# Kernel optimization log

Measured on AMD Instinct MI355X. Metric: run time of the kernel, lower is better.

## Reference

```python
import jax, jax.numpy as jnp
import numpy as np

B, T, C, H = 2, 2048, 2048, 16
DH = C // H  # 128
INNER = 4 * C  # 8192
EPS = 1e-5


def _ln(x, w, b):
    mu = jnp.mean(x, axis=-1, keepdims=True)
    var = jnp.mean((x - mu) ** 2, axis=-1, keepdims=True)
    return (x - mu) * jax.lax.rsqrt(var + EPS) * w + b


def _apply_rotary(x, cos, sin):
    # x: [B,H,T,DH]; cos/sin: [T,DH//2] broadcast over B,H
    x1 = x[..., ::2]
    x2 = x[..., 1::2]
    r = jnp.stack([x1 * cos - x2 * sin, x1 * sin + x2 * cos], axis=-1)
    return r.reshape(r.shape[:-2] + (-1,))


def setup_inputs() -> dict:
    key = jax.random.key(0)
    ks = jax.random.split(key, 8)
    std = 0.02
    x = jax.random.normal(ks[0], (B, T, C), dtype=jnp.float32)
    # RoPE tables
    inv_freq = 1.0 / (10000.0 ** (np.arange(0, DH, 2, dtype=np.float32) / DH))
    ang = np.arange(T, dtype=np.float32)[:, None] * inv_freq[None, :]  # [T, DH//2]
    cos = jnp.asarray(np.cos(ang))
    sin = jnp.asarray(np.sin(ang))
    return {
        "x": x,
        "cos": cos,
        "sin": sin,
        "ln1_w": jnp.ones((C,), jnp.float32),
        "ln1_b": jnp.zeros((C,), jnp.float32),
        "ln2_w": jnp.ones((C,), jnp.float32),
        "ln2_b": jnp.zeros((C,), jnp.float32),
        "W_qkv": jax.random.normal(ks[1], (C, 3 * C), jnp.float32) * std,
        "W_o": jax.random.normal(ks[2], (C, C), jnp.float32) * std,
        "W1": jax.random.normal(ks[3], (C, INNER), jnp.float32) * std,
        "W2": jax.random.normal(ks[4], (C, INNER), jnp.float32) * std,
        "W3": jax.random.normal(ks[5], (INNER, C), jnp.float32) * std,
    }


def reference(x, cos, sin, ln1_w, ln1_b, ln2_w, ln2_b, W_qkv, W_o, W1, W2, W3):
    # --- attention sub-block (pre-LN) ---
    a = _ln(x, ln1_w, ln1_b)
    qkv = a @ W_qkv  # [B,T,3C]
    q, k, v = jnp.split(qkv, 3, axis=-1)
    q = q.reshape(B, T, H, DH).transpose(0, 2, 1, 3)  # [B,H,T,DH]
    k = k.reshape(B, T, H, DH).transpose(0, 2, 1, 3)
    v = v.reshape(B, T, H, DH).transpose(0, 2, 1, 3)
    q = _apply_rotary(q, cos, sin)
    k = _apply_rotary(k, cos, sin)
    scores = jnp.einsum("bhtd,bhsd->bhts", q, k) / jnp.sqrt(jnp.float32(DH))
    mask = jnp.triu(jnp.full((T, T), -jnp.inf, dtype=scores.dtype), k=1)
    scores = scores + mask
    attn = jax.nn.softmax(scores, axis=-1)
    y = jnp.einsum("bhts,bhsd->bhtd", attn, v)
    y = y.transpose(0, 2, 1, 3).reshape(B, T, C) @ W_o
    x = x + y
    # --- SwiGLU MLP sub-block (pre-LN) ---
    h = _ln(x, ln2_w, ln2_b)
    m = (jax.nn.silu(h @ W1) * (h @ W2)) @ W3
    return x + m
```

## Files before the change

### kernel.cpp

```cpp
#include <hip/hip_runtime.h>
#include <hip/hip_bf16.h>
#include <cstdint>

#define DEVINL __device__ __forceinline__

using f32x4  = __attribute__((ext_vector_type(4))) float;
using short8 = __attribute__((ext_vector_type(8))) short;
using short4v = __attribute__((ext_vector_type(4))) short;

DEVINL float bf2f(__hip_bfloat16 h){ return __bfloat162float(h); }
DEVINL __hip_bfloat16 f2bf(float f){ return __float2bfloat16(f); }
DEVINL short bfbits(float f){ __hip_bfloat16 h = __float2bfloat16(f); short s; __builtin_memcpy(&s, &h, 2); return s; }
DEVINL float sb2f(short s){ uint32_t u = ((uint32_t)(uint16_t)s) << 16; float f; __builtin_memcpy(&f, &u, 4); return f; }

DEVINL void gl_lds16(const void* g, void* l){
  __builtin_amdgcn_global_load_lds((const __attribute__((address_space(1))) void*)g,
                                   (__attribute__((address_space(3))) void*)l, 16, 0, 0);
}

__global__ __launch_bounds__(256) void wtrans(const float* __restrict__ src,
                                              __hip_bfloat16* __restrict__ dst,
                                              int R, int C){
  __shared__ float tile[32][33];
  const int tr0 = blockIdx.y*32, tc0 = blockIdx.x*32;
  const int t = threadIdx.x;
  const int lr = t >> 3, lc = (t & 7) * 4;
  float4 v = *(const float4*)(src + (size_t)(tr0+lr)*C + tc0 + lc);
  tile[lr][lc] = v.x; tile[lr][lc+1] = v.y; tile[lr][lc+2] = v.z; tile[lr][lc+3] = v.w;
  __syncthreads();
  short4v o;
  o[0] = bfbits(tile[lc+0][lr]);
  o[1] = bfbits(tile[lc+1][lr]);
  o[2] = bfbits(tile[lc+2][lr]);
  o[3] = bfbits(tile[lc+3][lr]);
  *(short4v*)(dst + (size_t)(tc0+lr)*R + tr0 + lc) = o;
}

__global__ __launch_bounds__(256) void ln_k(const float* __restrict__ x,
                                            const float* __restrict__ w,
                                            const float* __restrict__ bia,
                                            __hip_bfloat16* __restrict__ out){
  const int row = blockIdx.x, t = threadIdx.x;
  const float* xr = x + (size_t)row*2048;
  float4 v0 = *(const float4*)(xr + t*4);
  float4 v1 = *(const float4*)(xr + 1024 + t*4);
  float s  = v0.x+v0.y+v0.z+v0.w + v1.x+v1.y+v1.z+v1.w;
  float ss = v0.x*v0.x+v0.y*v0.y+v0.z*v0.z+v0.w*v0.w
           + v1.x*v1.x+v1.y*v1.y+v1.z*v1.z+v1.w*v1.w;
  #pragma unroll
  for (int o=1;o<64;o<<=1){ s += __shfl_xor(s,o); ss += __shfl_xor(ss,o); }
  __shared__ float red[8];
  const int wv = t>>6, ln = t&63;
  if (ln==0){ red[wv]=s; red[4+wv]=ss; }
  __syncthreads();
  s = red[0]+red[1]+red[2]+red[3]; ss = red[4]+red[5]+red[6]+red[7];
  const float mu = s*(1.f/2048.f);
  const float inv = rsqrtf(ss*(1.f/2048.f) - mu*mu + 1e-5f);
  {
    float4 wv4 = *(const float4*)(w + t*4);
    float4 bv4 = *(const float4*)(bia + t*4);
    short4v o;
    o[0]=bfbits((v0.x-mu)*inv*wv4.x + bv4.x);
    o[1]=bfbits((v0.y-mu)*inv*wv4.y + bv4.y);
    o[2]=bfbits((v0.z-mu)*inv*wv4.z + bv4.z);
    o[3]=bfbits((v0.w-mu)*inv*wv4.w + bv4.w);
    *(short4v*)(out + (size_t)row*2048 + t*4) = o;
  }
  {
    float4 wv4 = *(const float4*)(w + 1024 + t*4);
    float4 bv4 = *(const float4*)(bia + 1024 + t*4);
    short4v o;
    o[0]=bfbits((v1.x-mu)*inv*wv4.x + bv4.x);
    o[1]=bfbits((v1.y-mu)*inv*wv4.y + bv4.y);
    o[2]=bfbits((v1.z-mu)*inv*wv4.z + bv4.z);
    o[3]=bfbits((v1.w-mu)*inv*wv4.w + bv4.w);
    *(short4v*)(out + (size_t)row*2048 + 1024 + t*4) = o;
  }
}

template<int EPI, int BM>
__global__ __launch_bounds__(512, 2) void gemmp(
    const __hip_bfloat16* __restrict__ A,
    const __hip_bfloat16* __restrict__ Bt,
    __hip_bfloat16* __restrict__ Cb,
    float* __restrict__ Cf,
    const float* __restrict__ resid,
    const __hip_bfloat16* __restrict__ emul,
    int M, int N, int K, int NTN)
{
  constexpr int MF    = BM/32;
  constexpr int LA    = BM/128;
  constexpr int ABY   = BM*64;
  constexpr int TILEB = ABY + 16384;
  extern __shared__ char smem[];
  const int tid = threadIdx.x, lane = tid & 63, wave = tid >> 6;
  const int l15 = lane & 15, l4 = lane >> 4;
  const int wm = wave >> 2, wn = wave & 3;

  const int nwg = gridDim.x;
  const int id  = blockIdx.x;
  const int swz = (id & 7) * (nwg >> 3) + (id >> 3);
  const int by = swz / NTN, bx = swz % NTN;
  const int row0 = by * BM, col0 = bx * 256;

  const __hip_bfloat16* srcA[LA]; int dstA[LA];
  #pragma unroll
  for (int g = 0; g < LA; ++g){
    const int c = g*512 + tid, r = c >> 2, s = c & 3;
    const int kbyte = (s*16) ^ (((r >> 1) & 3) << 4);
    srcA[g] = A + (size_t)(row0 + r)*K + (kbyte >> 1);
    dstA[g] = c*16;
  }
  const __hip_bfloat16* srcB[2]; int dstB[2];
  #pragma unroll
  for (int g = 0; g < 2; ++g){
    const int c = g*512 + tid, r = c >> 2, s = c & 3;
    const int kbyte = (s*16) ^ (((r >> 1) & 3) << 4);
    srcB[g] = Bt + (size_t)(col0 + r)*K + (kbyte >> 1);
    dstB[g] = c*16;
  }
  auto STAGE = [&](int bi, int kt){
    char* base = smem + bi*TILEB;
    #pragma unroll
    for (int g = 0; g < LA; ++g) gl_lds16(srcA[g] + kt*32, base + dstA[g]);
    #pragma unroll
    for (int g = 0; g < 2; ++g)  gl_lds16(srcB[g] + kt*32, base + ABY + dstB[g]);
  };

  const int rmask = ((l15 >> 1) & 3) << 4;
  int offA[MF], offB[4];
  #pragma unroll
  for (int m = 0; m < MF; ++m){
    const int r = wm*(BM/2) + m*16 + l15;
    offA[m] = r*64 + ((l4*16) ^ rmask);
  }
  #pragma unroll
  for (int n = 0; n < 4; ++n){
    const int r = wn*64 + n*16 + l15;
    offB[n] = r*64 + ((l4*16) ^ rmask);
  }

  f32x4 acc[MF][4] = {};
  const int NT = K >> 5;

  STAGE(0, 0); STAGE(1, 1); STAGE(2, 2);
  __builtin_amdgcn_sched_barrier(0);
  if constexpr (BM == 256) asm volatile("s_waitcnt vmcnt(8)" ::: "memory");
  else                     asm volatile("s_waitcnt vmcnt(6)" ::: "memory");
  __builtin_amdgcn_s_barrier();
  __builtin_amdgcn_sched_barrier(0);

  for (int t = 0; t < NT; ++t){
    const char* base = smem + (t & 3)*TILEB;
    if (t + 3 < NT) STAGE((t + 3) & 3, t + 3);
    short8 a[MF], b[4];
    #pragma unroll
    for (int m = 0; m < MF; ++m) a[m] = *(const short8*)(base + offA[m]);
    #pragma unroll
    for (int n = 0; n < 4; ++n)  b[n] = *(const short8*)(base + ABY + offB[n]);
    __builtin_amdgcn_s_setprio(1);
    #pragma unroll
    for (int m = 0; m < MF; ++m)
      #pragma unroll
      for (int n = 0; n < 4; ++n)
        acc[m][n] = __builtin_amdgcn_mfma_f32_16x16x32_bf16(a[m], b[n], acc[m][n], 0, 0, 0);
    __builtin_amdgcn_s_setprio(0);
    if (t + 3 < NT){
      if constexpr (BM == 256) asm volatile("s_waitcnt vmcnt(8)" ::: "memory");
      else                     asm volatile("s_waitcnt vmcnt(6)" ::: "memory");
    } else if (t + 2 < NT){
      if constexpr (BM == 256) asm volatile("s_waitcnt vmcnt(4)" ::: "memory");
      else                     asm volatile("s_waitcnt vmcnt(3)" ::: "memory");
    } else {
      asm volatile("s_waitcnt vmcnt(0)" ::: "memory");
    }
    __builtin_amdgcn_s_barrier();
    __builtin_amdgcn_sched_barrier(0);
  }

  #pragma unroll
  for (int m = 0; m < MF; ++m){
    const int r0 = row0 + wm*(BM/2) + m*16 + l4*4;
    #pragma unroll
    for (int n = 0; n < 4; ++n){
      const int c = col0 + wn*64 + n*16 + l15;
      #pragma unroll
      for (int j = 0; j < 4; ++j){
        const size_t idx = (size_t)(r0 + j)*N + c;
        const float v = acc[m][n][j];
        if constexpr (EPI == 1)      Cf[idx] = v + resid[idx];
        else if constexpr (EPI == 2) Cb[idx] = f2bf(v / (1.f + __expf(-v)));
        else if constexpr (EPI == 3) Cb[idx] = f2bf(v * bf2f(emul[idx]));
        else                         Cb[idx] = f2bf(v);
      }
    }
  }
}

__global__ __launch_bounds__(256) void ropepack(
    const __hip_bfloat16* __restrict__ qkv, const float* __restrict__ cosT, const float* __restrict__ sinT,
    __hip_bfloat16* __restrict__ Qo, __hip_bfloat16* __restrict__ Ko, __hip_bfloat16* __restrict__ Vo)
{
  __shared__ short vt[128][72];
  const int bh = blockIdx.y, b = bh>>4, h = bh&15;
  const int t0 = blockIdx.x*64, tid = threadIdx.x;
  const int tr = tid>>2, q4 = tid&3;
  const int tg = t0 + tr;
  const __hip_bfloat16* base = qkv + ((size_t)(b*2048 + tg))*6144 + h*128;
  const int pp0 = q4*16;
  float cs[16], sn[16];
  #pragma unroll
  for (int i=0;i<4;i++){
    float4 c4 = *(const float4*)(cosT + (size_t)tg*64 + pp0 + i*4);
    float4 s4 = *(const float4*)(sinT + (size_t)tg*64 + pp0 + i*4);
    cs[i*4+0]=c4.x; cs[i*4+1]=c4.y; cs[i*4+2]=c4.z; cs[i*4+3]=c4.w;
    sn[i*4+0]=s4.x; sn[i*4+1]=s4.y; sn[i*4+2]=s4.z; sn[i*4+3]=s4.w;
  }
  #pragma unroll
  for (int qk=0; qk<2; ++qk){
    const __hip_bfloat16* src = base + qk*2048;
    __hip_bfloat16* dst = (qk==0 ? Qo : Ko) + ((size_t)bh*2048 + tg)*128 + pp0*2;
    short8 ov[4];
    short* o = (short*)ov;
    #pragma unroll
    for (int i=0;i<4;i++){
      short8 v = *(const short8*)(src + pp0*2 + i*8);
      #pragma unroll
      for (int j=0;j<4;j++){
        float xe = sb2f(v[2*j]), xo = sb2f(v[2*j+1]);
        float c = cs[4*i+j], s = sn[4*i+j];
        o[8*i+2*j]   = bfbits(xe*c - xo*s);
        o[8*i+2*j+1] = bfbits(xe*s + xo*c);
      }
    }
    #pragma unroll
    for (int i=0;i<4;i++) *(short8*)(dst + i*8) = ov[i];
  }
  const __hip_bfloat16* vsrc = base + 4096;
  const int vc0 = q4*32;
  #pragma unroll
  for (int i=0;i<4;i++){
    short8 v = *(const short8*)(vsrc + vc0 + i*8);
    #pragma unroll
    for (int j=0;j<8;j++) vt[vc0+i*8+j][tr] = v[j];
  }
  __syncthreads();
  const int d = tid>>1, th0 = (tid&1)*32;
  __hip_bfloat16* vdst = Vo + ((size_t)bh*128 + d)*2048 + t0 + th0;
  #pragma unroll
  for (int i=0;i<4;i++)
    *(short8*)(vdst + i*8) = *(const short8*)(&vt[d][th0 + i*8]);
}

__global__ __launch_bounds__(512, 2) void attn_k(
    const __hip_bfloat16* __restrict__ Q,
    const __hip_bfloat16* __restrict__ K,
    const __hip_bfloat16* __restrict__ Vt,
    __hip_bfloat16* __restrict__ Y)
{
  extern __shared__ char lds[];
  const int bh = blockIdx.x, b = bh>>4, h = bh&15;
  const int by = blockIdx.y;
  const int qtA = 15 - 2*by, qtB = 2*by;
  const int tid = threadIdx.x, lane = tid&63, wave = tid>>6;
  const int qt = (wave < 4) ? qtA : qtB;
  const int qbase = qt*128 + (wave&3)*32;
  const int qmax = (qtA > qtB) ? qtA : qtB;
  const int nsteps = 2*qmax + 2;
  const __hip_bfloat16* Qh = Q + (size_t)bh*2048*128;
  const __hip_bfloat16* Kh = K + (size_t)bh*2048*128;
  const __hip_bfloat16* Vh = Vt + (size_t)bh*128*2048;
  char* plbase = lds + 65536 + wave*4608;
  const int l15 = lane & 15, l4 = lane >> 4;
  const int swzm = (l15 & 7) << 4;

  const int krA = tid >> 4;  const int kjA = (tid & 15) * 16;
  const size_t ksrcA = (size_t)krA*128 + ((kjA ^ ((krA & 7) << 4)) >> 1);
  const size_t ksrcB = (size_t)(krA+32)*128 + ((kjA ^ ((krA & 7) << 4)) >> 1);
  const int vrA = tid >> 3;  const int vjA = (tid & 7) * 16;
  const size_t vsrcA = (size_t)vrA*2048 + ((vjA ^ ((vrA & 7) << 4)) >> 1);
  const size_t vsrcB = (size_t)(vrA+64)*2048 + ((vjA ^ ((vrA & 7) << 4)) >> 1);
  auto STAGE = [&](int buf, int kv0){
    char* kb = lds + buf*16384;
    char* vb = lds + 32768 + buf*16384;
    gl_lds16(Kh + (size_t)kv0*128 + ksrcA, kb + tid*16);
    gl_lds16(Kh + (size_t)kv0*128 + ksrcB, kb + 8192 + tid*16);
    gl_lds16(Vh + kv0 + vsrcA, vb + tid*16);
    gl_lds16(Vh + kv0 + vsrcB, vb + 8192 + tid*16);
  };

  short8 qf[2][4];
  #pragma unroll
  for (int m=0;m<2;m++)
    #pragma unroll
    for (int kc=0;kc<4;kc++)
      qf[m][kc] = *(const short8*)(Qh + (size_t)(qbase + m*16 + l15)*128 + kc*32 + l4*8);

  short8 of;
  #pragma unroll
  for (int i=0;i<8;i++) of[i] = (l15==0) ? (short)0x3F80 : (short)0;

  f32x4 accO[2][9] = {};
  float mrow[2][4];
  #pragma unroll
  for (int m=0;m<2;m++)
    #pragma unroll
    for (int j=0;j<4;j++) mrow[m][j] = -1e30f;
  const float scale = 0.08838834764831845f;

  STAGE(0, 0);
  STAGE(1, 64);
  __builtin_amdgcn_sched_barrier(0);
  asm volatile("s_waitcnt vmcnt(4)" ::: "memory");
  __builtin_amdgcn_s_barrier();
  __builtin_amdgcn_sched_barrier(0);

  for (int s = 0; s < nsteps; ++s){
    const int kv0 = s*64;
    const char* kb = lds + (s&1)*16384;
    const char* vb = lds + 32768 + (s&1)*16384;
    if (kv0 <= qbase){
      const bool diag = (kv0 + 64 > qbase);
      const int kvrel = kv0 - qbase;
      f32x4 sc[2][4] = {};
      #pragma unroll
      for (int n=0;n<4;n++){
        short8 kf[4];
        #pragma unroll
        for (int kc=0;kc<4;kc++)
          kf[kc] = *(const short8*)(kb + (n*16 + l15)*256 + ((kc*64 + l4*16) ^ swzm));
        #pragma unroll
        for (int m=0;m<2;m++)
          #pragma unroll
          for (int kc=0;kc<4;kc++)
            sc[m][n] = __builtin_amdgcn_mfma_f32_16x16x32_bf16(qf[m][kc], kf[kc], sc[m][n], 0,0,0);
      }
      float alpha_[2][4];
      #pragma unroll
      for (int m=0;m<2;m++)
        #pragma unroll
        for (int j=0;j<4;j++){
          const int qr = 16*m + 4*l4 + j;
          float a[4];
          #pragma unroll
          for (int n=0;n<4;n++){
            a[n] = sc[m][n][j]*scale;
            if (diag && (kvrel + n*16 + l15 > qr)) a[n] = -1e30f;
          }
          float mx = fmaxf(fmaxf(a[0],a[1]), fmaxf(a[2],a[3]));
          #pragma unroll
          for (int o=1;o<16;o<<=1) mx = fmaxf(mx, __shfl_xor(mx, o));
          const float mn = fmaxf(mrow[m][j], mx);
          const float al = __expf(mrow[m][j] - mn);
          mrow[m][j] = mn;
          alpha_[m][j] = al;
          __hip_bfloat16* pr = (__hip_bfloat16*)(plbase + qr*144) + l15;
          #pragma unroll
          for (int n=0;n<4;n++) pr[n*16] = f2bf(__expf(a[n] - mn));
        }
      #pragma unroll
      for (int m=0;m<2;m++)
        #pragma unroll
        for (int db=0;db<9;db++)
          #pragma unroll
          for (int j=0;j<4;j++)
            accO[m][db][j] *= alpha_[m][j];
      asm volatile("s_waitcnt lgkmcnt(0)" ::: "memory");
      __builtin_amdgcn_sched_barrier(0);
      short8 pa[2][2];
      #pragma unroll
      for (int m=0;m<2;m++)
        #pragma unroll
        for (int ks=0;ks<2;ks++)
          pa[m][ks] = *(const short8*)(plbase + (m*16 + l15)*144 + ks*64 + l4*16);
      #pragma unroll
      for (int db=0;db<8;db++){
        #pragma unroll
        for (int ks=0;ks<2;ks++){
          short8 vf = *(const short8*)(vb + (db*16 + l15)*128 + ((ks*64 + l4*16) ^ swzm));
          #pragma unroll
          for (int m=0;m<2;m++)
            accO[m][db] = __builtin_amdgcn_mfma_f32_16x16x32_bf16(pa[m][ks], vf, accO[m][db], 0,0,0);
        }
      }
      #pragma unroll
      for (int ks=0;ks<2;ks++)
        #pragma unroll
        for (int m=0;m<2;m++)
          accO[m][8] = __builtin_amdgcn_mfma_f32_16x16x32_bf16(pa[m][ks], of, accO[m][8], 0,0,0);
    }
    __builtin_amdgcn_sched_barrier(0);
    __builtin_amdgcn_s_barrier();
    __builtin_amdgcn_sched_barrier(0);
    if (s + 2 < nsteps){
      STAGE(s&1, (s+2)*64);
      __builtin_amdgcn_sched_barrier(0);
      asm volatile("s_waitcnt vmcnt(4)" ::: "memory");
    } else {
      asm volatile("s_waitcnt vmcnt(0)" ::: "memory");
    }
    __builtin_amdgcn_s_barrier();
    __builtin_amdgcn_sched_barrier(0);
  }

  #pragma unroll
  for (int m=0;m<2;m++){
    float lr[4];
    #pragma unroll
    for (int j=0;j<4;j++) lr[j] = __shfl(accO[m][8][j], l4*16);
    #pragma unroll
    for (int db=0;db<8;db++)
      #pragma unroll
      for (int j=0;j<4;j++){
        const int tg = qbase + 16*m + 4*l4 + j;
        const int d  = 16*db + l15;
        Y[((size_t)b*2048 + tg)*2048 + h*128 + d] = f2bf(accO[m][db][j] / lr[j]);
      }
  }
}

extern "C" void kernel_launch(void* const* d_in, const int* in_sizes, int n_in,
                              void* d_out, int out_size, void* d_ws, size_t ws_size,
                              hipStream_t stream)
{
  const float* x    = (const float*)d_in[0];
  const float* cosT = (const float*)d_in[1];
  const float* sinT = (const float*)d_in[2];
  const float* ln1w = (const float*)d_in[3];
  const float* ln1b = (const float*)d_in[4];
  const float* ln2w = (const float*)d_in[5];
  const float* ln2b = (const float*)d_in[6];
  const float* Wqkv = (const float*)d_in[7];
  const float* Wo   = (const float*)d_in[8];
  const float* W1   = (const float*)d_in[9];
  const float* W2   = (const float*)d_in[10];
  const float* W3   = (const float*)d_in[11];
  float* out = (float*)d_out;

  if (ws_size < 150994944) return;
  char* ws = (char*)d_ws;
  __hip_bfloat16* WT   = (__hip_bfloat16*)(ws);
  __hip_bfloat16* abf  = (__hip_bfloat16*)(ws + 33554432);
  __hip_bfloat16* qkvb = (__hip_bfloat16*)(ws + 50331648);
  __hip_bfloat16* Yb   = (__hip_bfloat16*)(ws + 50331648);
  __hip_bfloat16* sub  = (__hip_bfloat16*)(ws + 50331648);
  __hip_bfloat16* Qb   = (__hip_bfloat16*)(ws + 100663296);
  __hip_bfloat16* Kb   = (__hip_bfloat16*)(ws + 117440512);
  __hip_bfloat16* Vtb  = (__hip_bfloat16*)(ws + 134217728);
  float*          x2   = out;

  hipFuncSetAttribute(reinterpret_cast<const void*>(&gemmp<4,128>),
                      hipFuncAttributeMaxDynamicSharedMemorySize, 98304);
  hipFuncSetAttribute(reinterpret_cast<const void*>(&gemmp<2,256>),
                      hipFuncAttributeMaxDynamicSharedMemorySize, 131072);
  hipFuncSetAttribute(reinterpret_cast<const void*>(&gemmp<3,256>),
                      hipFuncAttributeMaxDynamicSharedMemorySize, 131072);
  hipFuncSetAttribute(reinterpret_cast<const void*>(&gemmp<1,128>),
                      hipFuncAttributeMaxDynamicSharedMemorySize, 98304);
  hipFuncSetAttribute(reinterpret_cast<const void*>(&attn_k),
                      hipFuncAttributeMaxDynamicSharedMemorySize, 102400);

  ln_k<<<4096,256,0,stream>>>(x, ln1w, ln1b, abf);
  wtrans<<<dim3(192,64),256,0,stream>>>(Wqkv, WT, 2048, 6144);
  gemmp<4,128><<<768,512,98304,stream>>>(abf, WT, qkvb, nullptr, nullptr, nullptr, 4096, 6144, 2048, 24);
  ropepack<<<dim3(32,32),256,0,stream>>>(qkvb, cosT, sinT, Qb, Kb, Vtb);
  attn_k<<<dim3(32,8),512,102400,stream>>>(Qb, Kb, Vtb, Yb);
  wtrans<<<dim3(64,64),256,0,stream>>>(Wo, WT, 2048, 2048);
  gemmp<1,128><<<256,512,98304,stream>>>(Yb, WT, nullptr, x2, x, nullptr, 4096, 2048, 2048, 8);
  ln_k<<<4096,256,0,stream>>>(x2, ln2w, ln2b, abf);
  wtrans<<<dim3(256,64),256,0,stream>>>(W1, WT, 2048, 8192);
  gemmp<2,256><<<512,512,131072,stream>>>(abf, WT, sub, nullptr, nullptr, nullptr, 4096, 8192, 2048, 32);
  wtrans<<<dim3(256,64),256,0,stream>>>(W2, WT, 2048, 8192);
  gemmp<3,256><<<512,512,131072,stream>>>(abf, WT, sub, nullptr, nullptr, sub, 4096, 8192, 2048, 32);
  wtrans<<<dim3(64,256),256,0,stream>>>(W3, WT, 8192, 2048);
  gemmp<1,128><<<256,512,98304,stream>>>(sub, WT, nullptr, out, x2, nullptr, 4096, 2048, 8192, 8);
}
```

Before: 818.6 us.

## Fuse SwiGLU up/gate GEMMs into one dual-B kernel with silu-mul epilogue

```diff
diff --git a/kernel.cpp b/kernel.cpp
--- a/kernel.cpp
+++ b/kernel.cpp
@@ -192,6 +192,118 @@
         else if constexpr (EPI == 2) Cb[idx] = f2bf(v / (1.f + __expf(-v)));
         else if constexpr (EPI == 3) Cb[idx] = f2bf(v * bf2f(emul[idx]));
         else                         Cb[idx] = f2bf(v);
+      }
+    }
+  }
+}
+
+__global__ __launch_bounds__(512, 2) void gemmf(
+    const __hip_bfloat16* __restrict__ A,
+    const __hip_bfloat16* __restrict__ B1t,
+    const __hip_bfloat16* __restrict__ B2t,
+    __hip_bfloat16* __restrict__ Cb,
+    int M, int N, int K, int NTN)
+{
+  constexpr int ABY   = 16384;
+  constexpr int TILEB = ABY + 16384;
+  extern __shared__ char smem[];
+  const int tid = threadIdx.x, lane = tid & 63, wave = tid >> 6;
+  const int l15 = lane & 15, l4 = lane >> 4;
+  const int wm = wave >> 2, wn = wave & 3;
+
+  const int nwg = gridDim.x;
+  const int id  = blockIdx.x;
+  const int swz = (id & 7) * (nwg >> 3) + (id >> 3);
+  const int by = swz / NTN, bx = swz % NTN;
+  const int row0 = by * 256, col0 = bx * 128;
+
+  const __hip_bfloat16* srcA[2]; int dstA[2];
+  #pragma unroll
+  for (int g = 0; g < 2; ++g){
+    const int c = g*512 + tid, r = c >> 2, s = c & 3;
+    const int kbyte = (s*16) ^ (((r >> 1) & 3) << 4);
+    srcA[g] = A + (size_t)(row0 + r)*K + (kbyte >> 1);
+    dstA[g] = c*16;
+  }
+  const __hip_bfloat16* srcB[2]; int dstB[2];
+  #pragma unroll
+  for (int g = 0; g < 2; ++g){
+    const int c = g*512 + tid, r = c >> 2, s = c & 3;
+    const int kbyte = (s*16) ^ (((r >> 1) & 3) << 4);
+    const __hip_bfloat16* base = (r < 128) ? (B1t + (size_t)(col0 + r)*K)
+                                           : (B2t + (size_t)(col0 + r - 128)*K);
+    srcB[g] = base + (kbyte >> 1);
+    dstB[g] = c*16;
+  }
+  auto STAGE = [&](int bi, int kt){
+    char* base = smem + bi*TILEB;
+    #pragma unroll
+    for (int g = 0; g < 2; ++g) gl_lds16(srcA[g] + kt*32, base + dstA[g]);
+    #pragma unroll
+    for (int g = 0; g < 2; ++g) gl_lds16(srcB[g] + kt*32, base + ABY + dstB[g]);
+  };
+
+  const int rmask = ((l15 >> 1) & 3) << 4;
+  int offA[8], offB[2][2];
+  #pragma unroll
+  for (int m = 0; m < 8; ++m){
+    const int r = wm*128 + m*16 + l15;
+    offA[m] = r*64 + ((l4*16) ^ rmask);
+  }
+  #pragma unroll
+  for (int g = 0; g < 2; ++g)
+    #pragma unroll
+    for (int nf = 0; nf < 2; ++nf){
+      const int r = g*128 + wn*32 + nf*16 + l15;
+      offB[g][nf] = r*64 + ((l4*16) ^ rmask);
+    }
+
+  f32x4 acc[8][2][2] = {};
+  const int NT = K >> 5;
+
+  STAGE(0, 0); STAGE(1, 1); STAGE(2, 2);
+  __builtin_amdgcn_sched_barrier(0);
+  asm volatile("s_waitcnt vmcnt(8)" ::: "memory");
+  __builtin_amdgcn_s_barrier();
+  __builtin_amdgcn_sched_barrier(0);
+
+  for (int t = 0; t < NT; ++t){
+    const char* base = smem + (t & 3)*TILEB;
+    if (t + 3 < NT) STAGE((t + 3) & 3, t + 3);
+    short8 a[8], b[2][2];
+    #pragma unroll
+    for (int m = 0; m < 8; ++m) a[m] = *(const short8*)(base + offA[m]);
+    #pragma unroll
+    for (int g = 0; g < 2; ++g)
+      #pragma unroll
+      for (int nf = 0; nf < 2; ++nf) b[g][nf] = *(const short8*)(base + ABY + offB[g][nf]);
+    __builtin_amdgcn_s_setprio(1);
+    #pragma unroll
+    for (int m = 0; m < 8; ++m)
+      #pragma unroll
+      for (int g = 0; g < 2; ++g)
+        #pragma unroll
+        for (int nf = 0; nf < 2; ++nf)
+          acc[m][g][nf] = __builtin_amdgcn_mfma_f32_16x16x32_bf16(a[m], b[g][nf], acc[m][g][nf], 0, 0, 0);
+    __builtin_amdgcn_s_setprio(0);
+    if (t + 3 < NT)      asm volatile("s_waitcnt vmcnt(8)" ::: "memory");
+    else if (t + 2 < NT) asm volatile("s_waitcnt vmcnt(4)" ::: "memory");
+    else                 asm volatile("s_waitcnt vmcnt(0)" ::: "memory");
+    __builtin_amdgcn_s_barrier();
+    __builtin_amdgcn_sched_barrier(0);
+  }
+
+  #pragma unroll
+  for (int m = 0; m < 8; ++m){
+    const int r0 = row0 + wm*128 + m*16 + l4*4;
+    #pragma unroll
+    for (int nf = 0; nf < 2; ++nf){
+      const int c = col0 + wn*32 + nf*16 + l15;
+      #pragma unroll
+      for (int j = 0; j < 4; ++j){
+        const float h1 = acc[m][0][nf][j];
+        const float h2 = acc[m][1][nf][j];
+        Cb[(size_t)(r0 + j)*N + c] = f2bf((h1 / (1.f + __expf(-h1))) * h2);
       }
     }
   }
@@ -439,24 +551,24 @@
 
   if (ws_size < 150994944) return;
   char* ws = (char*)d_ws;
-  __hip_bfloat16* WT   = (__hip_bfloat16*)(ws);
-  __hip_bfloat16* abf  = (__hip_bfloat16*)(ws + 33554432);
-  __hip_bfloat16* qkvb = (__hip_bfloat16*)(ws + 50331648);
-  __hip_bfloat16* Yb   = (__hip_bfloat16*)(ws + 50331648);
-  __hip_bfloat16* sub  = (__hip_bfloat16*)(ws + 50331648);
-  __hip_bfloat16* Qb   = (__hip_bfloat16*)(ws + 100663296);
-  __hip_bfloat16* Kb   = (__hip_bfloat16*)(ws + 117440512);
-  __hip_bfloat16* Vtb  = (__hip_bfloat16*)(ws + 134217728);
-  float*          x2   = out;
+  __hip_bfloat16* WT    = (__hip_bfloat16*)(ws);
+  __hip_bfloat16* W2T   = (__hip_bfloat16*)(ws + 33554432);
+  __hip_bfloat16* WoT   = (__hip_bfloat16*)(ws + 50331648);
+  __hip_bfloat16* abf   = (__hip_bfloat16*)(ws + 67108864);
+  __hip_bfloat16* qkvb  = (__hip_bfloat16*)(ws + 83886080);
+  __hip_bfloat16* sub   = (__hip_bfloat16*)(ws + 83886080);
+  __hip_bfloat16* Qb    = (__hip_bfloat16*)(ws);
+  __hip_bfloat16* Kb    = (__hip_bfloat16*)(ws + 16777216);
+  __hip_bfloat16* Vtb   = (__hip_bfloat16*)(ws + 33554432);
+  __hip_bfloat16* Yb    = (__hip_bfloat16*)(ws + 134217728);
+  float*          x2    = out;
 
   hipFuncSetAttribute(reinterpret_cast<const void*>(&gemmp<4,128>),
                       hipFuncAttributeMaxDynamicSharedMemorySize, 98304);
-  hipFuncSetAttribute(reinterpret_cast<const void*>(&gemmp<2,256>),
-                      hipFuncAttributeMaxDynamicSharedMemorySize, 131072);
-  hipFuncSetAttribute(reinterpret_cast<const void*>(&gemmp<3,256>),
-                      hipFuncAttributeMaxDynamicSharedMemorySize, 131072);
   hipFuncSetAttribute(reinterpret_cast<const void*>(&gemmp<1,128>),
                       hipFuncAttributeMaxDynamicSharedMemorySize, 98304);
+  hipFuncSetAttribute(reinterpret_cast<const void*>(&gemmf),
+                      hipFuncAttributeMaxDynamicSharedMemorySize, 131072);
   hipFuncSetAttribute(reinterpret_cast<const void*>(&attn_k),
                       hipFuncAttributeMaxDynamicSharedMemorySize, 102400);
 
@@ -465,13 +577,12 @@
   gemmp<4,128><<<768,512,98304,stream>>>(abf, WT, qkvb, nullptr, nullptr, nullptr, 4096, 6144, 2048, 24);
   ropepack<<<dim3(32,32),256,0,stream>>>(qkvb, cosT, sinT, Qb, Kb, Vtb);
   attn_k<<<dim3(32,8),512,102400,stream>>>(Qb, Kb, Vtb, Yb);
-  wtrans<<<dim3(64,64),256,0,stream>>>(Wo, WT, 2048, 2048);
-  gemmp<1,128><<<256,512,98304,stream>>>(Yb, WT, nullptr, x2, x, nullptr, 4096, 2048, 2048, 8);
+  wtrans<<<dim3(64,64),256,0,stream>>>(Wo, WoT, 2048, 2048);
+  gemmp<1,128><<<256,512,98304,stream>>>(Yb, WoT, nullptr, x2, x, nullptr, 4096, 2048, 2048, 8);
   ln_k<<<4096,256,0,stream>>>(x2, ln2w, ln2b, abf);
   wtrans<<<dim3(256,64),256,0,stream>>>(W1, WT, 2048, 8192);
-  gemmp<2,256><<<512,512,131072,stream>>>(abf, WT, sub, nullptr, nullptr, nullptr, 4096, 8192, 2048, 32);
-  wtrans<<<dim3(256,64),256,0,stream>>>(W2, WT, 2048, 8192);
-  gemmp<3,256><<<512,512,131072,stream>>>(abf, WT, sub, nullptr, nullptr, sub, 4096, 8192, 2048, 32);
+  wtrans<<<dim3(256,64),256,0,stream>>>(W2, W2T, 2048, 8192);
+  gemmf<<<1024,512,131072,stream>>>(abf, WT, W2T, sub, 4096, 8192, 2048, 64);
   wtrans<<<dim3(64,256),256,0,stream>>>(W3, WT, 8192, 2048);
   gemmp<1,128><<<256,512,98304,stream>>>(sub, WT, nullptr, out, x2, nullptr, 4096, 2048, 8192, 8);
 }
```

Result: faster. 796.3 us (-2.7%).

## Add 256x256 eight-phase pipelined GEMM for QKV and SwiGLU projections

Applied to the files above, without the earlier changes.

```diff
diff --git a/kernel.cpp b/kernel.cpp
--- a/kernel.cpp
+++ b/kernel.cpp
@@ -190,6 +190,134 @@
         const float v = acc[m][n][j];
         if constexpr (EPI == 1)      Cf[idx] = v + resid[idx];
         else if constexpr (EPI == 2) Cb[idx] = f2bf(v / (1.f + __expf(-v)));
+        else if constexpr (EPI == 3) Cb[idx] = f2bf(v * bf2f(emul[idx]));
+        else                         Cb[idx] = f2bf(v);
+      }
+    }
+  }
+}
+
+#define G8_PHASE(BUF, MH, NH, READB, SDSTOFF, SBASE, SKT, VM) do {                          \
+  const char* bb_ = smem + (BUF)*65536;                                                     \
+  short8 afr[4][2];                                                                         \
+  _Pragma("unroll")                                                                         \
+  for (int m_=0;m_<4;m_++){                                                                 \
+    _Pragma("unroll")                                                                       \
+    for (int k_=0;k_<2;k_++) afr[m_][k_] = *(const short8*)(bb_ + offA[(MH)*4+m_][k_]); }   \
+  if (READB){                                                                               \
+    _Pragma("unroll")                                                                       \
+    for (int n_=0;n_<2;n_++){                                                               \
+      _Pragma("unroll")                                                                     \
+      for (int k_=0;k_<2;k_++) bfr[n_][k_] = *(const short8*)(bb_ + offB[(NH)*2+n_][k_]); } } \
+  STG((SDSTOFF), (SBASE), (SKT));                                                           \
+  if (VM) asm volatile("s_waitcnt vmcnt(4)" ::: "memory");                                  \
+  __builtin_amdgcn_s_barrier();                                                             \
+  asm volatile("s_waitcnt lgkmcnt(0)" ::: "memory");                                        \
+  __builtin_amdgcn_sched_barrier(0);                                                        \
+  __builtin_amdgcn_s_setprio(1);                                                            \
+  _Pragma("unroll")                                                                         \
+  for (int m_=0;m_<4;m_++){                                                                 \
+    _Pragma("unroll")                                                                       \
+    for (int n_=0;n_<2;n_++){                                                               \
+      _Pragma("unroll")                                                                     \
+      for (int k_=0;k_<2;k_++)                                                              \
+        acc[(MH)*4+m_][(NH)*2+n_] = __builtin_amdgcn_mfma_f32_16x16x32_bf16(                \
+            afr[m_][k_], bfr[n_][k_], acc[(MH)*4+m_][(NH)*2+n_], 0,0,0); } }                \
+  __builtin_amdgcn_s_setprio(0);                                                            \
+  __builtin_amdgcn_s_barrier();                                                             \
+  __builtin_amdgcn_sched_barrier(0);                                                        \
+} while(0)
+
+template<int EPI>
+__global__ __launch_bounds__(512, 2) void gemm8x(
+    const __hip_bfloat16* __restrict__ A,
+    const __hip_bfloat16* __restrict__ Bt,
+    __hip_bfloat16* __restrict__ Cb,
+    const __hip_bfloat16* __restrict__ emul,
+    int M, int N, int K, int NTN)
+{
+  extern __shared__ char smem[];
+  const int tid = threadIdx.x, lane = tid & 63, wave = tid >> 6;
+  const int l15 = lane & 15, l4 = lane >> 4;
+  const int wm = wave >> 2, wn = wave & 3;
+
+  const int nwg = gridDim.x;
+  const int id  = blockIdx.x;
+  const int swz = (id & 7) * (nwg >> 3) + (id >> 3);
+  const int by = swz / NTN, bx = swz % NTN;
+  const int row0 = by * 256, col0 = bx * 256;
+
+  const __hip_bfloat16* pAlo = A  + (size_t)row0*K;
+  const __hip_bfloat16* pAhi = A  + (size_t)(row0+128)*K;
+  const __hip_bfloat16* pBlo = Bt + (size_t)col0*K;
+  const __hip_bfloat16* pBhi = Bt + (size_t)(col0+128)*K;
+
+  const int c0r = tid >> 3, c0s = tid & 7;
+  const size_t so0 = (size_t)c0r*K + (((c0s*16) ^ ((c0r & 7) << 4)) >> 1);
+  const int c1 = 512 + tid, c1r = c1 >> 3, c1s = c1 & 7;
+  const size_t so1 = (size_t)c1r*K + (((c1s*16) ^ ((c1r & 7) << 4)) >> 1);
+  const int do0 = tid*16, do1 = c1*16;
+  auto STG = [&](int dstoff, const __hip_bfloat16* base, int kt){
+    gl_lds16(base + (size_t)kt*64 + so0, smem + dstoff + do0);
+    gl_lds16(base + (size_t)kt*64 + so1, smem + dstoff + do1);
+  };
+
+  int offA[8][2], offB[4][2];
+  #pragma unroll
+  for (int m = 0; m < 8; ++m){
+    const int row = wm*128 + m*16 + l15;
+    const int part = row >> 7, rr = row & 127;
+    #pragma unroll
+    for (int ks = 0; ks < 2; ++ks)
+      offA[m][ks] = part*16384 + rr*128 + ((ks*64 + l4*16) ^ ((rr & 7) << 4));
+  }
+  #pragma unroll
+  for (int n = 0; n < 4; ++n){
+    const int row = wn*64 + n*16 + l15;
+    const int part = row >> 7, rr = row & 127;
+    #pragma unroll
+    for (int ks = 0; ks < 2; ++ks)
+      offB[n][ks] = 32768 + part*16384 + rr*128 + ((ks*64 + l4*16) ^ ((rr & 7) << 4));
+  }
+
+  f32x4 acc[8][4] = {};
+  short8 bfr[2][2];
+  const int NT = K >> 6, NITER = NT >> 1;
+
+  STG(0,         pAlo, 0); STG(16384,       pAhi, 0);
+  STG(32768,     pBlo, 0); STG(49152,       pBhi, 0);
+  STG(65536+32768, pBlo, 1); STG(65536+0,   pAlo, 1);
+  __builtin_amdgcn_sched_barrier(0);
+  asm volatile("s_waitcnt vmcnt(4)" ::: "memory");
+  __builtin_amdgcn_s_barrier();
+  __builtin_amdgcn_sched_barrier(0);
+
+  for (int i = 0; i < NITER; ++i){
+    const int T0 = 2*i;
+    const int s01 = T0 + 1;
+    const int s02 = (T0+2 < NT) ? T0+2 : 0;
+    const int s03 = (T0+3 < NT) ? T0+3 : 0;
+    G8_PHASE(0, 0,0, true,  65536+16384, pAhi, s01, 0);
+    G8_PHASE(0, 1,0, false, 65536+49152, pBhi, s01, 0);
+    G8_PHASE(0, 0,1, true,  0+32768,     pBlo, s02, 0);
+    G8_PHASE(0, 1,1, false, 0+0,         pAlo, s02, 1);
+    G8_PHASE(1, 0,0, true,  0+16384,     pAhi, s02, 0);
+    G8_PHASE(1, 1,0, false, 0+49152,     pBhi, s02, 0);
+    G8_PHASE(1, 0,1, true,  65536+32768, pBlo, s03, 0);
+    G8_PHASE(1, 1,1, false, 65536+0,     pAlo, s03, 1);
+  }
+
+  #pragma unroll
+  for (int m = 0; m < 8; ++m){
+    const int r0 = row0 + wm*128 + m*16 + l4*4;
+    #pragma unroll
+    for (int n = 0; n < 4; ++n){
+      const int c = col0 + wn*64 + n*16 + l15;
+      #pragma unroll
+      for (int j = 0; j < 4; ++j){
+        const size_t idx = (size_t)(r0 + j)*N + c;
+        const float v = acc[m][n][j];
+        if constexpr (EPI == 2)      Cb[idx] = f2bf(v / (1.f + __expf(-v)));
         else if constexpr (EPI == 3) Cb[idx] = f2bf(v * bf2f(emul[idx]));
         else                         Cb[idx] = f2bf(v);
       }
@@ -439,21 +567,23 @@
 
   if (ws_size < 150994944) return;
   char* ws = (char*)d_ws;
-  __hip_bfloat16* WT   = (__hip_bfloat16*)(ws);
-  __hip_bfloat16* abf  = (__hip_bfloat16*)(ws + 33554432);
-  __hip_bfloat16* qkvb = (__hip_bfloat16*)(ws + 50331648);
-  __hip_bfloat16* Yb   = (__hip_bfloat16*)(ws + 50331648);
-  __hip_bfloat16* sub  = (__hip_bfloat16*)(ws + 50331648);
-  __hip_bfloat16* Qb   = (__hip_bfloat16*)(ws + 100663296);
-  __hip_bfloat16* Kb   = (__hip_bfloat16*)(ws + 117440512);
-  __hip_bfloat16* Vtb  = (__hip_bfloat16*)(ws + 134217728);
-  float*          x2   = out;
-
-  hipFuncSetAttribute(reinterpret_cast<const void*>(&gemmp<4,128>),
-                      hipFuncAttributeMaxDynamicSharedMemorySize, 98304);
-  hipFuncSetAttribute(reinterpret_cast<const void*>(&gemmp<2,256>),
+  __hip_bfloat16* WT    = (__hip_bfloat16*)(ws);
+  __hip_bfloat16* W2T   = (__hip_bfloat16*)(ws + 33554432);
+  __hip_bfloat16* WoT   = (__hip_bfloat16*)(ws + 50331648);
+  __hip_bfloat16* abf   = (__hip_bfloat16*)(ws + 67108864);
+  __hip_bfloat16* qkvb  = (__hip_bfloat16*)(ws + 83886080);
+  __hip_bfloat16* sub   = (__hip_bfloat16*)(ws + 83886080);
+  __hip_bfloat16* Qb    = (__hip_bfloat16*)(ws);
+  __hip_bfloat16* Kb    = (__hip_bfloat16*)(ws + 16777216);
+  __hip_bfloat16* Vtb   = (__hip_bfloat16*)(ws + 33554432);
+  __hip_bfloat16* Yb    = (__hip_bfloat16*)(ws + 134217728);
+  float*          x2    = out;
+
+  hipFuncSetAttribute(reinterpret_cast<const void*>(&gemm8x<4>),
                       hipFuncAttributeMaxDynamicSharedMemorySize, 131072);
-  hipFuncSetAttribute(reinterpret_cast<const void*>(&gemmp<3,256>),
+  hipFuncSetAttribute(reinterpret_cast<const void*>(&gemm8x<2>),
+                      hipFuncAttributeMaxDynamicSharedMemorySize, 131072);
+  hipFuncSetAttribute(reinterpret_cast<const void*>(&gemm8x<3>),
                       hipFuncAttributeMaxDynamicSharedMemorySize, 131072);
   hipFuncSetAttribute(reinterpret_cast<const void*>(&gemmp<1,128>),
                       hipFuncAttributeMaxDynamicSharedMemorySize, 98304);
@@ -462,16 +592,16 @@
 
   ln_k<<<4096,256,0,stream>>>(x, ln1w, ln1b, abf);
   wtrans<<<dim3(192,64),256,0,stream>>>(Wqkv, WT, 2048, 6144);
-  gemmp<4,128><<<768,512,98304,stream>>>(abf, WT, qkvb, nullptr, nullptr, nullptr, 4096, 6144, 2048, 24);
+  gemm8x<4><<<384,512,131072,stream>>>(abf, WT, qkvb, nullptr, 4096, 6144, 2048, 24);
   ropepack<<<dim3(32,32),256,0,stream>>>(qkvb, cosT, sinT, Qb, Kb, Vtb);
   attn_k<<<dim3(32,8),512,102400,stream>>>(Qb, Kb, Vtb, Yb);
-  wtrans<<<dim3(64,64),256,0,stream>>>(Wo, WT, 2048, 2048);
-  gemmp<1,128><<<256,512,98304,stream>>>(Yb, WT, nullptr, x2, x, nullptr, 4096, 2048, 2048, 8);
+  wtrans<<<dim3(64,64),256,0,stream>>>(Wo, WoT, 2048, 2048);
+  gemmp<1,128><<<256,512,98304,stream>>>(Yb, WoT, nullptr, x2, x, nullptr, 4096, 2048, 2048, 8);
   ln_k<<<4096,256,0,stream>>>(x2, ln2w, ln2b, abf);
   wtrans<<<dim3(256,64),256,0,stream>>>(W1, WT, 2048, 8192);
-  gemmp<2,256><<<512,512,131072,stream>>>(abf, WT, sub, nullptr, nullptr, nullptr, 4096, 8192, 2048, 32);
-  wtrans<<<dim3(256,64),256,0,stream>>>(W2, WT, 2048, 8192);
-  gemmp<3,256><<<512,512,131072,stream>>>(abf, WT, sub, nullptr, nullptr, sub, 4096, 8192, 2048, 32);
+  gemm8x<2><<<512,512,131072,stream>>>(abf, WT, sub, nullptr, 4096, 8192, 2048, 32);
+  wtrans<<<dim3(256,64),256,0,stream>>>(W2, W2T, 2048, 8192);
+  gemm8x<3><<<512,512,131072,stream>>>(abf, W2T, sub, sub, 4096, 8192, 2048, 32);
   wtrans<<<dim3(64,256),256,0,stream>>>(W3, WT, 8192, 2048);
   gemmp<1,128><<<256,512,98304,stream>>>(sub, WT, nullptr, out, x2, nullptr, 4096, 2048, 8192, 8);
 }
```

Result: no change. 815.0 us (-0.4%).
